# Performance work log

Hardware: AMD Instinct MI355X
Metric: run time of the kernel (lower is better)

## Reference

```python
import jax, jax.numpy as jnp
import numpy as np

CHANNELS = 512
GROUPS = 32
EPS = 1e-5


def setup_inputs() -> dict:
    key = jax.random.key(0)
    ks = jax.random.split(key, 7)
    C = CHANNELS
    x = jax.random.normal(ks[0], (32, C, 32, 32), dtype=jnp.float32)
    norm_w = jax.random.normal(ks[1], (C,), dtype=jnp.float32) * 0.02 + 1.0
    norm_b = jax.random.normal(ks[2], (C,), dtype=jnp.float32) * 0.02
    # 1x1 convs stored as (out_channels, in_channels)
    qkv_w = jax.random.normal(ks[3], (3 * C, C), dtype=jnp.float32) * (C ** -0.5)
    qkv_b = jax.random.normal(ks[4], (3 * C,), dtype=jnp.float32) * 0.02
    proj_w = jax.random.normal(ks[5], (C, C), dtype=jnp.float32) * (C ** -0.5)
    proj_b = jax.random.normal(ks[6], (C,), dtype=jnp.float32) * 0.02
    return {"x": x, "norm_w": norm_w, "norm_b": norm_b,
            "qkv_w": qkv_w, "qkv_b": qkv_b,
            "proj_w": proj_w, "proj_b": proj_b}


def _group_norm(x, w, b):
    B, C, H, W = x.shape
    xg = x.reshape(B, GROUPS, C // GROUPS, H, W)
    mean = xg.mean(axis=(2, 3, 4), keepdims=True)
    var = xg.var(axis=(2, 3, 4), keepdims=True)
    xn = ((xg - mean) * jax.lax.rsqrt(var + EPS)).reshape(B, C, H, W)
    return xn * w[None, :, None, None] + b[None, :, None, None]


def reference(x, norm_w, norm_b, qkv_w, qkv_b, proj_w, proj_b):
    B, C, H, W = x.shape
    scale = C ** (-0.5)
    h = _group_norm(x, norm_w, norm_b)
    # 1x1 conv == per-pixel linear: (B,C,H,W) -> (B,3C,H,W)
    qkv = jnp.einsum('bchw,oc->bohw', h, qkv_w) + qkv_b[None, :, None, None]
    qkv = qkv.reshape(B, 3, C, H * W)
    q, k, v = qkv[:, 0], qkv[:, 1], qkv[:, 2]  # each (B, C, N)
    # attn[b, i, j] = softmax_j( q[:, i] . k[:, j] * scale )
    scores = jnp.einsum('bcn,bcm->bnm', q, k) * scale  # (B, N, N)
    attn = jax.nn.softmax(scores, axis=-1)
    # h[b, c, i] = sum_j v[b, c, j] * attn[b, i, j]
    hout = jnp.einsum('bcm,bnm->bcn', v, attn).reshape(B, C, H, W)
    out = x + jnp.einsum('bchw,oc->bohw', hout, proj_w) + proj_b[None, :, None, None]
    return out
```

## Files before the change

### kernel.cpp

```cpp
#include <hip/hip_runtime.h>
#include <math.h>

#define B_ 32
#define C_ 512
#define G_ 32
#define N_ 1024
#define OC3_ 1536
#define EPS_ 1e-5f

typedef __attribute__((ext_vector_type(8))) short short8;
typedef __attribute__((ext_vector_type(4))) float f32x4;

__device__ inline unsigned short f2bf(float f) {
    unsigned u = __builtin_bit_cast(unsigned, f);
    u += 0x7fffu + ((u >> 16) & 1u);
    return (unsigned short)(u >> 16);
}
__device__ inline unsigned pack2(float lo, float hi) {
    return (unsigned)f2bf(lo) | ((unsigned)f2bf(hi) << 16);
}
__device__ inline float bf2f(unsigned short u) {
    return __builtin_bit_cast(float, ((unsigned)u) << 16);
}

typedef const __attribute__((address_space(1))) unsigned int* gas_u32;
typedef __attribute__((address_space(3))) unsigned int* las_u32;
__device__ __forceinline__ void cp16(unsigned short* lds, const unsigned short* g) {
    __builtin_amdgcn_global_load_lds((gas_u32)g, (las_u32)lds, 16, 0, 0);
}

__device__ __forceinline__ void xcd_decode(int bid, int nbpb, int nbz,
                                           int& bz, int& local) {
    if ((nbz & 7) == 0) {
        int xcd = bid & 7;
        int rest = bid >> 3;
        local = rest % nbpb;
        bz = (rest / nbpb) * 8 + xcd;
    } else {
        bz = bid / nbpb;
        local = bid % nbpb;
    }
}

__global__ __launch_bounds__(256) void gn_stats_kernel(
    const float* __restrict__ x, float* __restrict__ stats)
{
    int bg = blockIdx.x;
    const float4* xv = (const float4*)(x + (size_t)bg * 16 * N_);
    float s = 0.f, ss = 0.f;
    for (int i = threadIdx.x; i < 4096; i += 256) {
        float4 v = xv[i];
        s  += v.x + v.y + v.z + v.w;
        ss += v.x*v.x + v.y*v.y + v.z*v.z + v.w*v.w;
    }
    __shared__ float r1[256], r2[256];
    r1[threadIdx.x] = s; r2[threadIdx.x] = ss;
    __syncthreads();
    for (int off = 128; off > 0; off >>= 1) {
        if (threadIdx.x < off) {
            r1[threadIdx.x] += r1[threadIdx.x + off];
            r2[threadIdx.x] += r2[threadIdx.x + off];
        }
        __syncthreads();
    }
    if (threadIdx.x == 0) {
        float mean = r1[0] * (1.f / 16384.f);
        float var  = r2[0] * (1.f / 16384.f) - mean * mean;
        stats[bg * 2 + 0] = mean;
        stats[bg * 2 + 1] = rsqrtf(var + EPS_);
    }
}

__global__ __launch_bounds__(256) void cvt_bf16_kernel(
    const float* __restrict__ src, unsigned short* __restrict__ dst, int n4)
{
    int i = blockIdx.x * 256 + threadIdx.x;
    if (i >= n4) return;
    float4 v = ((const float4*)src)[i];
    uint2 o; o.x = pack2(v.x, v.y); o.y = pack2(v.z, v.w);
    ((uint2*)dst)[i] = o;
}

__global__ __launch_bounds__(256) void hhatT_kernel(
    const float* __restrict__ x, const float* __restrict__ stats,
    const float* __restrict__ nw, const float* __restrict__ nbias,
    unsigned short* __restrict__ hhatT, long sH, int b0, int nbz)
{
    int bz, local;
    xcd_decode(blockIdx.x, 128, nbz, bz, local);
    int b = b0 + bz;
    int nt = (local & 15) * 64, ct = (local >> 4) * 64;
    const float* xb = x + (size_t)b * C_ * N_;
    const float* st = stats + b * 2 * G_;

    __shared__ float T[64][65];
    int tid = threadIdx.x;

    #pragma unroll
    for (int p = 0; p < 4; ++p) {
        int c = p * 16 + (tid >> 4);
        int n4 = (tid & 15) * 4;
        float4 v = *(const float4*)&xb[(size_t)(ct + c) * N_ + nt + n4];
        int g = (ct + c) >> 4;
        float w0 = nw[ct + c] * st[g * 2 + 1];
        float bb = nbias[ct + c] - st[g * 2] * w0;
        T[c][n4]   = v.x * w0 + bb;
        T[c][n4+1] = v.y * w0 + bb;
        T[c][n4+2] = v.z * w0 + bb;
        T[c][n4+3] = v.w * w0 + bb;
    }
    __syncthreads();
    #pragma unroll
    for (int p = 0; p < 2; ++p) {
        int n  = p * 32 + (tid >> 3);
        int c8 = (tid & 7) * 8;
        short8 s;
        #pragma unroll
        for (int u = 0; u < 8; ++u) s[u] = (short)f2bf(T[c8 + u][n]);
        *(short8*)&hhatT[(size_t)bz * sH + (size_t)(nt + n) * C_ + ct + c8] = s;
    }
}

template<int EPI>
__global__ __launch_bounds__(256) void gemm128(
    const unsigned short* __restrict__ A, long sA, int lda,
    const unsigned short* __restrict__ B, long sB, int ldb,
    void* __restrict__ Dv, long sD, int ldd,
    const float* __restrict__ bias,
    const float* __restrict__ aux, long sAux,
    int K, float scale, int gx, int gy, int nbz)
{
    int bz, local;
    xcd_decode(blockIdx.x, gx * gy, nbz, bz, local);

    int bx, by;
    bool p2 = false;
    if constexpr (EPI == 5) {
        p2 = local >= 64;
        int li = p2 ? local - 64 : local;
        bx = p2 ? (li & 3) : (li & 7);
        by = p2 ? (li >> 2) : (li >> 3);
    } else {
        bx = local % gx;
        by = local / gx;
    }

    const unsigned short *Ab, *Bb;
    if constexpr (EPI == 5) {
        if (p2) {
            Ab = B + (size_t)(1024 + bx * 128) * ldb;
            Bb = A + (size_t)bz * sA + (size_t)by * 128 * lda;
        } else {
            Ab = A + (size_t)bz * sA + (size_t)bx * 128 * lda;
            Bb = B + (size_t)by * 128 * ldb;
        }
    } else {
        Ab = A + (size_t)bz * sA + (size_t)bx * 128 * lda;
        Bb = B + (size_t)bz * sB + (size_t)by * 128 * ldb;
    }

    __shared__ __align__(16) unsigned short smem[4][4096];

    int tid = threadIdx.x;
    int w = tid >> 6, lane = tid & 63;
    int lm = lane & 15, q = lane >> 4;
    int wrow = (w >> 1) * 64, wcol = (w & 1) * 64;

    f32x4 acc[4][4];
    #pragma unroll
    for (int i = 0; i < 4; ++i)
        #pragma unroll
        for (int j = 0; j < 4; ++j) acc[i][j] = (f32x4)(0.f);

    int srow = tid >> 2;
    int skc  = (((tid & 3) ^ ((tid >> 3) & 3))) * 8;
    int fco  = (q ^ ((lm >> 1) & 3)) * 8;

    const unsigned short* a0p = Ab + (size_t)srow        * lda + skc;
    const unsigned short* a1p = Ab + (size_t)(64 + srow) * lda + skc;
    const unsigned short* b0p = Bb + (size_t)srow        * ldb + skc;
    const unsigned short* b1p = Bb + (size_t)(64 + srow) * ldb + skc;

    cp16(&smem[0][tid * 8],        a0p);
    cp16(&smem[0][2048 + tid * 8], a1p);
    cp16(&smem[2][tid * 8],        b0p);
    cp16(&smem[2][2048 + tid * 8], b1p);

    int nIter = K >> 5;
    for (int it = 0; it < nIter; ++it) {
        int cur = it & 1;
        __syncthreads();
        if (it + 1 < nIter) {
            int off = (it + 1) * 32;
            int nxt = cur ^ 1;
            cp16(&smem[nxt][tid * 8],            a0p + off);
            cp16(&smem[nxt][2048 + tid * 8],     a1p + off);
            cp16(&smem[2 + nxt][tid * 8],        b0p + off);
            cp16(&smem[2 + nxt][2048 + tid * 8], b1p + off);
        }
        short8 af[4], bf[4];
        #pragma unroll
        for (int i = 0; i < 4; ++i)
            af[i] = *(const short8*)&smem[cur][(wrow + i * 16 + lm) * 32 + fco];
        #pragma unroll
        for (int j = 0; j < 4; ++j)
            bf[j] = *(const short8*)&smem[2 + cur][(wcol + j * 16 + lm) * 32 + fco];
        #pragma unroll
        for (int i = 0; i < 4; ++i)
            #pragma unroll
            for (int j = 0; j < 4; ++j)
                acc[i][j] = __builtin_amdgcn_mfma_f32_16x16x32_bf16(
                    af[i], bf[j], acc[i][j], 0, 0, 0);
    }

    __syncthreads();

    if constexpr (EPI != 4) {
        unsigned short* Ts = &smem[0][0];
        #pragma unroll
        for (int j = 0; j < 4; ++j) {
            int lc = wcol + j * 16 + lm;
            float cb = 0.f;
            if constexpr (EPI == 5) { if (!p2) cb = bias[by * 128 + lc]; }
            #pragma unroll
            for (int i = 0; i < 4; ++i) {
                #pragma unroll
                for (int r = 0; r < 4; ++r) {
                    int lr = wrow + i * 16 + q * 4 + r;
                    float vle = acc[i][j][r];
                    if constexpr (EPI == 2) vle *= scale;
                    else if constexpr (EPI == 5)
                        vle += p2 ? bias[1024 + bx * 128 + lr] : cb;
                    int wkey = (lr >> 2) & 7;
                    Ts[lr * 128 + (lc ^ (wkey << 3))] = f2bf(vle);
                }
            }
        }
        __syncthreads();
        size_t doff = 0;
        if constexpr (EPI == 5) { if (p2) doff = (size_t)(1u << 20); }
        unsigned short* Dp = (unsigned short*)Dv + doff +
            (size_t)bz * sD + (size_t)(bx * 128) * ldd + by * 128;
        #pragma unroll
        for (int k = 0; k < 8; ++k) {
            int flat = k * 2048 + tid * 8;
            int rr = flat >> 7, cc = flat & 127;
            int key = (rr >> 2) & 7;
            short8 vv = *(const short8*)&Ts[flat ^ (key << 3)];
            *(short8*)&Dp[(size_t)rr * ldd + cc] = vv;
        }
    } else {
        float* Ts32 = (float*)&smem[0][0];
        float* Dp = (float*)Dv + (size_t)bz * sD + (size_t)(bx * 128) * ldd + by * 128;
        const float* Ap = aux + (size_t)bz * sAux + (size_t)(bx * 128) * ldd + by * 128;
        #pragma unroll
        for (int h = 0; h < 2; ++h) {
            if (h) __syncthreads();
            if ((w & 1) == h) {
                #pragma unroll
                for (int j = 0; j < 4; ++j) {
                    int lch = j * 16 + lm;
                    #pragma unroll
                    for (int i = 0; i < 4; ++i) {
                        #pragma unroll
                        for (int r = 0; r < 4; ++r) {
                            int lr = wrow + i * 16 + q * 4 + r;
                            int wkey = (lr >> 2) & 7;
                            Ts32[lr * 64 + (lch ^ (wkey << 3))] =
                                acc[i][j][r] + bias[bx * 128 + lr];
                        }
                    }
                }
            }
            __syncthreads();
            #pragma unroll
            for (int k = 0; k < 8; ++k) {
                int flat = k * 1024 + tid * 4;
                int rr = flat >> 6, cc = flat & 63;
                int key = (rr >> 2) & 7;
                f32x4 vv = *(const f32x4*)&Ts32[flat ^ (key << 3)];
                size_t go = (size_t)rr * ldd + h * 64 + cc;
                f32x4 av = *(const f32x4*)&Ap[go];
                *(f32x4*)&Dp[go] = vv + av;
            }
        }
    }
}

__global__ __launch_bounds__(256) void softmax_kernel(
    unsigned short* __restrict__ sc, long sSc, int nbz)
{
    int bz, local;
    xcd_decode(blockIdx.x, 256, nbz, bz, local);
    int row = local * 4 + (threadIdx.x >> 6);
    int lane = threadIdx.x & 63;
    unsigned short* p = sc + (size_t)bz * sSc + (size_t)row * N_ + lane * 16;

    short8 s0 = *(const short8*)p;
    short8 s1 = *(const short8*)(p + 8);
    float v[16];
    #pragma unroll
    for (int i = 0; i < 8; ++i) {
        v[i]     = bf2f((unsigned short)s0[i]);
        v[8 + i] = bf2f((unsigned short)s1[i]);
    }
    float m = v[0];
    #pragma unroll
    for (int i = 1; i < 16; ++i) m = fmaxf(m, v[i]);
    #pragma unroll
    for (int off = 32; off > 0; off >>= 1) m = fmaxf(m, __shfl_xor(m, off, 64));

    float sum = 0.f;
    #pragma unroll
    for (int i = 0; i < 16; ++i) { v[i] = __expf(v[i] - m); sum += v[i]; }
    #pragma unroll
    for (int off = 32; off > 0; off >>= 1) sum += __shfl_xor(sum, off, 64);
    float inv = 1.f / sum;

    short8 o0, o1;
    #pragma unroll
    for (int i = 0; i < 8; ++i) {
        o0[i] = (short)f2bf(v[i] * inv);
        o1[i] = (short)f2bf(v[8 + i] * inv);
    }
    *(short8*)p = o0;
    *(short8*)(p + 8) = o1;
}

extern "C" void kernel_launch(void* const* d_in, const int* in_sizes, int n_in,
                              void* d_out, int out_size, void* d_ws, size_t ws_size,
                              hipStream_t stream) {
    const float* x      = (const float*)d_in[0];
    const float* norm_w = (const float*)d_in[1];
    const float* norm_b = (const float*)d_in[2];
    const float* qkv_w  = (const float*)d_in[3];
    const float* qkv_b  = (const float*)d_in[4];
    const float* proj_w = (const float*)d_in[5];
    const float* proj_b = (const float*)d_in[6];
    float* out = (float*)d_out;

    char* ws = (char*)d_ws;
    float* stats = (float*)ws;
    unsigned short* wqkv  = (unsigned short*)(ws + 8192);
    unsigned short* wproj = wqkv + (size_t)OC3_ * C_;
    char* base = (char*)(wproj + (size_t)C_ * C_);
    const size_t fixed = 8192 + (size_t)OC3_ * C_ * 2 + (size_t)C_ * C_ * 2;

    const size_t REG = 6u << 20;
    const long RSH = (long)(REG / 2);

    size_t avail = ws_size > fixed ? ws_size - fixed : 0;
    int chunk = (int)(avail / REG);
    if (chunk < 1) chunk = 1;
    if (chunk > B_) chunk = B_;

    gn_stats_kernel<<<dim3(B_ * G_), dim3(256), 0, stream>>>(x, stats);
    cvt_bf16_kernel<<<dim3((OC3_ * C_ / 4 + 255) / 256), dim3(256), 0, stream>>>(
        qkv_w, wqkv, OC3_ * C_ / 4);
    cvt_bf16_kernel<<<dim3((C_ * C_ / 4 + 255) / 256), dim3(256), 0, stream>>>(
        proj_w, wproj, C_ * C_ / 4);

    const float scale = 0.044194173824159216f;

    unsigned short* qkT   = (unsigned short*)base;
    unsigned short* vbuf  = (unsigned short*)(base + (2u << 20));
    unsigned short* hhatT = (unsigned short*)(base + (3u << 20));
    unsigned short* houtT = (unsigned short*)(base + (3u << 20));
    unsigned short* sc    = (unsigned short*)(base + (4u << 20));

    for (int b0 = 0; b0 < B_; b0 += chunk) {
        int nb = B_ - b0 < chunk ? B_ - b0 : chunk;

        hhatT_kernel<<<dim3(128 * nb), dim3(256), 0, stream>>>(
            x, stats, norm_w, norm_b, hhatT, RSH, b0, nb);

        gemm128<5><<<dim3(96 * nb), dim3(256), 0, stream>>>(
            hhatT, RSH, C_,  wqkv, 0, C_,
            qkT, RSH, 1024,  qkv_b, nullptr, 0, C_, 0.f, 96, 1, nb);

        gemm128<2><<<dim3(8 * 8 * nb), dim3(256), 0, stream>>>(
            qkT, RSH, 1024,  qkT + 512, RSH, 1024,
            sc, RSH, N_,  nullptr, nullptr, 0, C_, scale, 8, 8, nb);

        softmax_kernel<<<dim3(256 * nb), dim3(256), 0, stream>>>(sc, RSH, nb);

        gemm128<3><<<dim3(8 * 4 * nb), dim3(256), 0, stream>>>(
            sc, RSH, N_,  vbuf, RSH, N_,
            houtT, RSH, C_,  nullptr, nullptr, 0, N_, 0.f, 8, 4, nb);

        gemm128<4><<<dim3(4 * 8 * nb), dim3(256), 0, stream>>>(
            wproj, 0, C_,  houtT, RSH, C_,
            out + (size_t)b0 * C_ * N_, (long)C_ * N_, N_,
            proj_b, x + (size_t)b0 * C_ * N_, (long)C_ * N_, C_, 0.f, 4, 8, nb);
    }
}
```

Measured before the change: 385.2 us.

## Merge prep kernels, deepen GEMM K-step to 64, simplify epilogue swizzle

Fuses the group-norm statistics kernel and both weight bf16 conversions into a single launch. The GEMM now loads two 32-wide K slabs per iteration, so each barrier covers 64 of K and twice as many MFMAs. This doubles shared memory to 64 KB and may lower occupancy. The epilogue LDS transpose swizzle keys are also changed to simpler per-lane and per-wave XOR patterns to reduce bank conflicts.

```diff
diff --git a/kernel.cpp b/kernel.cpp
--- a/kernel.cpp
+++ b/kernel.cpp
@@ -42,43 +42,53 @@
     }
 }
 
-__global__ __launch_bounds__(256) void gn_stats_kernel(
-    const float* __restrict__ x, float* __restrict__ stats)
+__global__ __launch_bounds__(256) void prep_kernel(
+    const float* __restrict__ x, float* __restrict__ stats,
+    const float* __restrict__ qkv_w, unsigned short* __restrict__ wqkv,
+    const float* __restrict__ proj_w, unsigned short* __restrict__ wproj)
 {
-    int bg = blockIdx.x;
-    const float4* xv = (const float4*)(x + (size_t)bg * 16 * N_);
-    float s = 0.f, ss = 0.f;
-    for (int i = threadIdx.x; i < 4096; i += 256) {
-        float4 v = xv[i];
-        s  += v.x + v.y + v.z + v.w;
-        ss += v.x*v.x + v.y*v.y + v.z*v.z + v.w*v.w;
-    }
     __shared__ float r1[256], r2[256];
-    r1[threadIdx.x] = s; r2[threadIdx.x] = ss;
-    __syncthreads();
-    for (int off = 128; off > 0; off >>= 1) {
-        if (threadIdx.x < off) {
-            r1[threadIdx.x] += r1[threadIdx.x + off];
-            r2[threadIdx.x] += r2[threadIdx.x + off];
-        }
+    int bid = blockIdx.x;
+    if (bid < 1024) {
+        int bg = bid;
+        const float4* xv = (const float4*)(x + (size_t)bg * 16 * N_);
+        float s = 0.f, ss = 0.f;
+        for (int i = threadIdx.x; i < 4096; i += 256) {
+            float4 v = xv[i];
+            s  += v.x + v.y + v.z + v.w;
+            ss += v.x*v.x + v.y*v.y + v.z*v.z + v.w*v.w;
+        }
+        r1[threadIdx.x] = s; r2[threadIdx.x] = ss;
         __syncthreads();
-    }
-    if (threadIdx.x == 0) {
-        float mean = r1[0] * (1.f / 16384.f);
-        float var  = r2[0] * (1.f / 16384.f) - mean * mean;
-        stats[bg * 2 + 0] = mean;
-        stats[bg * 2 + 1] = rsqrtf(var + EPS_);
-    }
-}
-
-__global__ __launch_bounds__(256) void cvt_bf16_kernel(
-    const float* __restrict__ src, unsigned short* __restrict__ dst, int n4)
-{
-    int i = blockIdx.x * 256 + threadIdx.x;
-    if (i >= n4) return;
-    float4 v = ((const float4*)src)[i];
-    uint2 o; o.x = pack2(v.x, v.y); o.y = pack2(v.z, v.w);
-    ((uint2*)dst)[i] = o;
+        for (int off = 128; off > 0; off >>= 1) {
+            if (threadIdx.x < off) {
+                r1[threadIdx.x] += r1[threadIdx.x + off];
+                r2[threadIdx.x] += r2[threadIdx.x + off];
+            }
+            __syncthreads();
+        }
+        if (threadIdx.x == 0) {
+            float mean = r1[0] * (1.f / 16384.f);
+            float var  = r2[0] * (1.f / 16384.f) - mean * mean;
+            stats[bg * 2 + 0] = mean;
+            stats[bg * 2 + 1] = rsqrtf(var + EPS_);
+        }
+    } else {
+        int i = (bid - 1024) * 256 + threadIdx.x;
+        const int nQ = OC3_ * C_ / 4;
+        float4 v;
+        uint2 o;
+        if (i < nQ) {
+            v = ((const float4*)qkv_w)[i];
+            o.x = pack2(v.x, v.y); o.y = pack2(v.z, v.w);
+            ((uint2*)wqkv)[i] = o;
+        } else {
+            int j = i - nQ;
+            v = ((const float4*)proj_w)[j];
+            o.x = pack2(v.x, v.y); o.y = pack2(v.z, v.w);
+            ((uint2*)wproj)[j] = o;
+        }
+    }
 }
 
 __global__ __launch_bounds__(256) void hhatT_kernel(
@@ -159,7 +169,7 @@
         Bb = B + (size_t)bz * sB + (size_t)by * 128 * ldb;
     }
 
-    __shared__ __align__(16) unsigned short smem[4][4096];
+    __shared__ __align__(16) unsigned short smem[8][4096];
 
     int tid = threadIdx.x;
     int w = tid >> 6, lane = tid & 63;
@@ -181,36 +191,51 @@
     const unsigned short* b0p = Bb + (size_t)srow        * ldb + skc;
     const unsigned short* b1p = Bb + (size_t)(64 + srow) * ldb + skc;
 
-    cp16(&smem[0][tid * 8],        a0p);
-    cp16(&smem[0][2048 + tid * 8], a1p);
-    cp16(&smem[2][tid * 8],        b0p);
-    cp16(&smem[2][2048 + tid * 8], b1p);
-
-    int nIter = K >> 5;
+    {
+        cp16(&smem[0][tid * 8],        a0p);
+        cp16(&smem[0][2048 + tid * 8], a1p);
+        cp16(&smem[1][tid * 8],        a0p + 32);
+        cp16(&smem[1][2048 + tid * 8], a1p + 32);
+        cp16(&smem[4][tid * 8],        b0p);
+        cp16(&smem[4][2048 + tid * 8], b1p);
+        cp16(&smem[5][tid * 8],        b0p + 32);
+        cp16(&smem[5][2048 + tid * 8], b1p + 32);
+    }
+
+    int nIter = K >> 6;
     for (int it = 0; it < nIter; ++it) {
         int cur = it & 1;
         __syncthreads();
         if (it + 1 < nIter) {
-            int off = (it + 1) * 32;
+            int off = (it + 1) * 64;
             int nxt = cur ^ 1;
-            cp16(&smem[nxt][tid * 8],            a0p + off);
-            cp16(&smem[nxt][2048 + tid * 8],     a1p + off);
-            cp16(&smem[2 + nxt][tid * 8],        b0p + off);
-            cp16(&smem[2 + nxt][2048 + tid * 8], b1p + off);
-        }
-        short8 af[4], bf[4];
-        #pragma unroll
-        for (int i = 0; i < 4; ++i)
-            af[i] = *(const short8*)&smem[cur][(wrow + i * 16 + lm) * 32 + fco];
-        #pragma unroll
-        for (int j = 0; j < 4; ++j)
-            bf[j] = *(const short8*)&smem[2 + cur][(wcol + j * 16 + lm) * 32 + fco];
-        #pragma unroll
-        for (int i = 0; i < 4; ++i)
+            cp16(&smem[nxt * 2][tid * 8],            a0p + off);
+            cp16(&smem[nxt * 2][2048 + tid * 8],     a1p + off);
+            cp16(&smem[nxt * 2 + 1][tid * 8],        a0p + off + 32);
+            cp16(&smem[nxt * 2 + 1][2048 + tid * 8], a1p + off + 32);
+            cp16(&smem[4 + nxt * 2][tid * 8],            b0p + off);
+            cp16(&smem[4 + nxt * 2][2048 + tid * 8],     b1p + off);
+            cp16(&smem[4 + nxt * 2 + 1][tid * 8],        b0p + off + 32);
+            cp16(&smem[4 + nxt * 2 + 1][2048 + tid * 8], b1p + off + 32);
+        }
+        #pragma unroll
+        for (int s = 0; s < 2; ++s) {
+            const unsigned short* As = smem[cur * 2 + s];
+            const unsigned short* Bs = smem[4 + cur * 2 + s];
+            short8 af[4], bf[4];
+            #pragma unroll
+            for (int i = 0; i < 4; ++i)
+                af[i] = *(const short8*)&As[(wrow + i * 16 + lm) * 32 + fco];
             #pragma unroll
             for (int j = 0; j < 4; ++j)
-                acc[i][j] = __builtin_amdgcn_mfma_f32_16x16x32_bf16(
-                    af[i], bf[j], acc[i][j], 0, 0, 0);
+                bf[j] = *(const short8*)&Bs[(wcol + j * 16 + lm) * 32 + fco];
+            #pragma unroll
+            for (int i = 0; i < 4; ++i)
+                #pragma unroll
+                for (int j = 0; j < 4; ++j)
+                    acc[i][j] = __builtin_amdgcn_mfma_f32_16x16x32_bf16(
+                        af[i], bf[j], acc[i][j], 0, 0, 0);
+        }
     }
 
     __syncthreads();
@@ -231,8 +256,7 @@
                     if constexpr (EPI == 2) vle *= scale;
                     else if constexpr (EPI == 5)
                         vle += p2 ? bias[1024 + bx * 128 + lr] : cb;
-                    int wkey = (lr >> 2) & 7;
-                    Ts[lr * 128 + (lc ^ (wkey << 3))] = f2bf(vle);
+                    Ts[lr * 128 + (lc ^ (q << 4))] = f2bf(vle);
                 }
             }
         }
@@ -245,8 +269,7 @@
         for (int k = 0; k < 8; ++k) {
             int flat = k * 2048 + tid * 8;
             int rr = flat >> 7, cc = flat & 127;
-            int key = (rr >> 2) & 7;
-            short8 vv = *(const short8*)&Ts[flat ^ (key << 3)];
+            short8 vv = *(const short8*)&Ts[flat ^ (w << 4)];
             *(short8*)&Dp[(size_t)rr * ldd + cc] = vv;
         }
     } else {
@@ -277,7 +300,7 @@
             for (int k = 0; k < 8; ++k) {
                 int flat = k * 1024 + tid * 4;
                 int rr = flat >> 6, cc = flat & 63;
-                int key = (rr >> 2) & 7;
+                int key = (4 * k + w) & 7;
                 f32x4 vv = *(const f32x4*)&Ts32[flat ^ (key << 3)];
                 size_t go = (size_t)rr * ldd + h * 64 + cc;
                 f32x4 av = *(const f32x4*)&Ap[go];
@@ -354,11 +377,8 @@
     if (chunk < 1) chunk = 1;
     if (chunk > B_) chunk = B_;
 
-    gn_stats_kernel<<<dim3(B_ * G_), dim3(256), 0, stream>>>(x, stats);
-    cvt_bf16_kernel<<<dim3((OC3_ * C_ / 4 + 255) / 256), dim3(256), 0, stream>>>(
-        qkv_w, wqkv, OC3_ * C_ / 4);
-    cvt_bf16_kernel<<<dim3((C_ * C_ / 4 + 255) / 256), dim3(256), 0, stream>>>(
-        proj_w, wproj, C_ * C_ / 4);
+    prep_kernel<<<dim3(2048), dim3(256), 0, stream>>>(
+        x, stats, qkv_w, wqkv, proj_w, wproj);
 
     const float scale = 0.044194173824159216f;
 
```

After: 373.4 us. 1.03x faster.
